# Kernel optimization log

Hardware: AMD Instinct MI355X
Metric: run time of the kernel (lower is better)

The kernel has to match this reference:

```python
import jax, jax.numpy as jnp
import numpy as np

N_SITES = 16
BATCH = 8192
K = 256
EPS = 1e-10


def _entanglement_entropy(sites_A, sites_B):
    # sites_A: [b, pA, k], sites_B: [b, pB, k]
    corr = jnp.einsum('bik,bjk->bij', sites_A, sites_B)  # [b, pA, pB]
    s = jnp.linalg.svd(corr, compute_uv=False)           # [b, min(pA,pB)]
    s_sq = s * s + EPS
    p = s_sq / jnp.sum(s_sq, axis=-1, keepdims=True)
    return -jnp.sum(p * jnp.log(p + EPS), axis=-1)        # [b]


def setup_inputs() -> dict:
    key = jax.random.key(0)
    sites = jax.random.normal(key, (BATCH, N_SITES, K), dtype=jnp.float32)
    return {"sites": sites}


def reference(sites) -> jnp.ndarray:
    # sites: [batch, n_sites, k]; list-of-tensors in the original, stacked here.
    n = sites.shape[1]
    mid = n // 2  # 8
    # Whole-system bipartition
    S_whole = _entanglement_entropy(sites[:, :mid], sites[:, mid:])
    # Left half bipartition (mid_left = mid // 2 = 4)
    ml = mid // 2
    S_left = _entanglement_entropy(sites[:, :ml], sites[:, ml:mid])
    # Right half bipartition
    nr = n - mid
    mr = nr // 2
    S_right = _entanglement_entropy(sites[:, mid:mid + mr], sites[:, mid + mr:])
    phi_q = S_whole - (S_left + S_right)
    return jax.nn.relu(phi_q)
```

## Files before the change

### kernel.cpp

```cpp
#include <hip/hip_runtime.h>
#include <math.h>

#define DEV __device__ __forceinline__

DEV float rcp_fast(float x) { return __builtin_amdgcn_rcpf(x); }
DEV float rsq_fast(float x) { return __builtin_amdgcn_rsqf(x); }

__host__ __device__ constexpr int TI(int n, int i, int j) {
  return n * i - (i * (i - 1)) / 2 + (j - i);
}

template <int N>
DEV float& sym_at(float (&a)[N * (N + 1) / 2], int i, int j) {
  return (i <= j) ? a[TI(N, i, j)] : a[TI(N, j, i)];
}

template <int N>
DEV void pivot_params(float (&a)[N * (N + 1) / 2], int p, int q,
                      float& c_out, float& s_out) {
  float apq = a[TI(N, p, q)];
  float app = a[TI(N, p, p)];
  float aqq = a[TI(N, q, q)];
  float h = aqq - app;
  float tw = apq + apq;
  float den = fabsf(h) + sqrtf(fmaf(h, h, tw * tw)) + 1e-37f;
  float t = tw * rcp_fast(den);
  t = (h < 0.0f) ? -t : t;
  float c = rsq_fast(fmaf(t, t, 1.0f));
  float s = t * c;
  c_out = c;
  s_out = s;
  a[TI(N, p, p)] = fmaf(-t, apq, app);
  a[TI(N, q, q)] = fmaf( t, apq, aqq);
  a[TI(N, p, q)] = 0.0f;
}

template <int N>
DEV void cross_update(float (&a)[N * (N + 1) / 2], int pa, int qa, int pb,
                      int qb, float ca, float sa, float cb, float sb) {
  float w = sym_at<N>(a, pa, pb), x = sym_at<N>(a, pa, qb);
  float y = sym_at<N>(a, qa, pb), z = sym_at<N>(a, qa, qb);
  float w1 = fmaf(ca, w, -sa * y), x1 = fmaf(ca, x, -sa * z);
  float y1 = fmaf(sa, w,  ca * y), z1 = fmaf(sa, x,  ca * z);
  sym_at<N>(a, pa, pb) = fmaf(cb, w1, -sb * x1);
  sym_at<N>(a, pa, qb) = fmaf(sb, w1,  cb * x1);
  sym_at<N>(a, qa, pb) = fmaf(cb, y1, -sb * z1);
  sym_at<N>(a, qa, qb) = fmaf(sb, y1,  cb * z1);
}

template <int SW8, int SW4>
DEV void jacobi_fused(float (&W)[36], float (&L)[10], float (&R)[10]) {
  constexpr int P8[7][4][2] = {
      {{0, 7}, {1, 6}, {2, 5}, {3, 4}}, {{0, 1}, {2, 7}, {3, 6}, {4, 5}},
      {{0, 2}, {1, 3}, {4, 7}, {5, 6}}, {{0, 3}, {2, 4}, {1, 5}, {6, 7}},
      {{0, 4}, {3, 5}, {2, 6}, {1, 7}}, {{0, 5}, {4, 6}, {3, 7}, {1, 2}},
      {{0, 6}, {5, 7}, {1, 4}, {2, 3}}};
  constexpr int P4[3][2][2] = {
      {{0, 3}, {1, 2}}, {{0, 1}, {2, 3}}, {{0, 2}, {1, 3}}};
#pragma unroll
  for (int rr = 0; rr < SW8 * 7; ++rr) {
    const int r = rr % 7;
    const bool do4 = ((rr & 1) == 0) && ((rr >> 1) < SW4 * 3);
    const int q = (rr >> 1) % 3;

    float cc[4], ss[4];
#pragma unroll
    for (int u = 0; u < 4; ++u)
      pivot_params<8>(W, P8[r][u][0], P8[r][u][1], cc[u], ss[u]);

    float ca0, sa0, ca1, sa1, cb0, sb0, cb1, sb1;
    if (do4) {
      pivot_params<4>(L, P4[q][0][0], P4[q][0][1], ca0, sa0);
      pivot_params<4>(R, P4[q][0][0], P4[q][0][1], cb0, sb0);
      pivot_params<4>(L, P4[q][1][0], P4[q][1][1], ca1, sa1);
      pivot_params<4>(R, P4[q][1][0], P4[q][1][1], cb1, sb1);
    }

#pragma unroll
    for (int u = 0; u < 4; ++u) {
#pragma unroll
      for (int v = u + 1; v < 4; ++v) {
        cross_update<8>(W, P8[r][u][0], P8[r][u][1], P8[r][v][0], P8[r][v][1],
                        cc[u], ss[u], cc[v], ss[v]);
      }
    }

    if (do4) {
      cross_update<4>(L, P4[q][0][0], P4[q][0][1], P4[q][1][0], P4[q][1][1],
                      ca0, sa0, ca1, sa1);
      cross_update<4>(R, P4[q][0][0], P4[q][0][1], P4[q][1][0], P4[q][1][1],
                      cb0, sb0, cb1, sb1);
    }
  }
}

template <int N>
DEV float entropy_of(const float (&a)[N * (N + 1) / 2]) {
  float lam[N];
  float sum = 0.0f;
#pragma unroll
  for (int i = 0; i < N; ++i) {
    float l = fmaxf(a[TI(N, i, i)], 0.0f) + 1e-10f;
    lam[i] = l;
    sum += l;
  }
  float inv = 1.0f / sum;
  float H = 0.0f;
#pragma unroll
  for (int i = 0; i < N; ++i) {
    float p = lam[i] * inv;
    H = fmaf(p, __logf(p + 1e-10f), H);
  }
  return -H;
}

DEV float reduce_dist_64(float (&cur)[64], int lane) {
#pragma unroll
  for (int d = 0; d < 6; ++d) {
    const int dist = 1 << d;
    const int up = (lane >> d) & 1;
#pragma unroll
    for (int m = 0; m < (64 >> (d + 1)); ++m) {
      float snd = up ? cur[2 * m]     : cur[2 * m + 1];
      float kp  = up ? cur[2 * m + 1] : cur[2 * m];
      float r = __shfl_xor(snd, dist, 64);
      cur[m] = kp + r;
    }
  }
  return cur[0];
}

DEV float reduce_dist_32(float (&cur)[32], int lane) {
#pragma unroll
  for (int d = 0; d < 5; ++d) {
    const int dist = 1 << d;
    const int up = (lane >> d) & 1;
#pragma unroll
    for (int m = 0; m < (32 >> (d + 1)); ++m) {
      float snd = up ? cur[2 * m]     : cur[2 * m + 1];
      float kp  = up ? cur[2 * m + 1] : cur[2 * m];
      float r = __shfl_xor(snd, dist, 64);
      cur[m] = kp + r;
    }
  }
  float v = cur[0];
  v += __shfl_xor(v, 32, 64);
  return v;
}

__global__ __launch_bounds__(64) void corr_kernel(
    const float* __restrict__ sites, float* __restrict__ cmat) {
  const int b = blockIdx.x;
  const int lane = threadIdx.x;
  const float4* base = reinterpret_cast<const float4*>(sites) + (size_t)b * 1024;

  float4 v[16];
#pragma unroll
  for (int s = 0; s < 16; ++s) v[s] = base[s * 64 + lane];

  float aw[64];
#pragma unroll
  for (int i = 0; i < 8; ++i) {
#pragma unroll
    for (int j = 0; j < 8; ++j) {
      float4 a = v[i], c = v[8 + j];
      aw[i * 8 + j] =
          fmaf(a.x, c.x, fmaf(a.y, c.y, fmaf(a.z, c.z, a.w * c.w)));
    }
  }
  float cw = reduce_dist_64(aw, lane);

  float alr[32];
#pragma unroll
  for (int i = 0; i < 4; ++i) {
#pragma unroll
    for (int j = 0; j < 4; ++j) {
      float4 a = v[i], c = v[4 + j];
      alr[i * 4 + j] =
          fmaf(a.x, c.x, fmaf(a.y, c.y, fmaf(a.z, c.z, a.w * c.w)));
      float4 a2 = v[8 + i], c2 = v[12 + j];
      alr[16 + i * 4 + j] =
          fmaf(a2.x, c2.x, fmaf(a2.y, c2.y, fmaf(a2.z, c2.z, a2.w * c2.w)));
    }
  }
  float clr = reduce_dist_32(alr, lane);

  float* row = cmat + (size_t)b * 96;
  row[lane] = cw;
  if (lane < 32) row[64 + lane] = clr;
}

__global__ __launch_bounds__(64) void phi_kernel(
    const float* __restrict__ cmat, float* __restrict__ out) {
  __shared__ float4 lds[64 * 25];
  const int t = threadIdx.x;
  const int b0 = blockIdx.x * 64;

  const float4* src = reinterpret_cast<const float4*>(cmat) + (size_t)b0 * 24;
#pragma unroll
  for (int r = 0; r < 24; ++r) {
    int q = r * 64 + t;
    float4 val = src[q];
    int bl = q / 24;
    int e4 = q - bl * 24;
    lds[bl * 25 + e4] = val;
  }
  __syncthreads();

  const float4* myrow = &lds[t * 25];
  float Cw[64], Cl[16], Cr[16];
#pragma unroll
  for (int j = 0; j < 16; ++j) {
    float4 f = myrow[j];
    Cw[4 * j] = f.x; Cw[4 * j + 1] = f.y; Cw[4 * j + 2] = f.z; Cw[4 * j + 3] = f.w;
  }
#pragma unroll
  for (int j = 0; j < 4; ++j) {
    float4 f = myrow[16 + j];
    Cl[4 * j] = f.x; Cl[4 * j + 1] = f.y; Cl[4 * j + 2] = f.z; Cl[4 * j + 3] = f.w;
    float4 g = myrow[20 + j];
    Cr[4 * j] = g.x; Cr[4 * j + 1] = g.y; Cr[4 * j + 2] = g.z; Cr[4 * j + 3] = g.w;
  }

  float Mw[36];
#pragma unroll
  for (int i = 0; i < 8; ++i) {
#pragma unroll
    for (int j = i; j < 8; ++j) {
      float acc = 0.0f;
#pragma unroll
      for (int k = 0; k < 8; ++k) acc = fmaf(Cw[i * 8 + k], Cw[j * 8 + k], acc);
      Mw[TI(8, i, j)] = acc;
    }
  }
  float Ml[10], Mr[10];
#pragma unroll
  for (int i = 0; i < 4; ++i) {
#pragma unroll
    for (int j = i; j < 4; ++j) {
      float accl = 0.0f, accr = 0.0f;
#pragma unroll
      for (int k = 0; k < 4; ++k) {
        accl = fmaf(Cl[i * 4 + k], Cl[j * 4 + k], accl);
        accr = fmaf(Cr[i * 4 + k], Cr[j * 4 + k], accr);
      }
      Ml[TI(4, i, j)] = accl;
      Mr[TI(4, i, j)] = accr;
    }
  }

  jacobi_fused<3, 3>(Mw, Ml, Mr);

  float Sw = entropy_of<8>(Mw);
  float Sl = entropy_of<4>(Ml);
  float Sr = entropy_of<4>(Mr);

  out[b0 + t] = fmaxf(Sw - Sl - Sr, 0.0f);
}

extern "C" void kernel_launch(void* const* d_in, const int* in_sizes, int n_in,
                              void* d_out, int out_size, void* d_ws, size_t ws_size,
                              hipStream_t stream) {
  const float* sites = (const float*)d_in[0];
  float* out = (float*)d_out;
  float* cmat = (float*)d_ws;

  corr_kernel<<<8192, 64, 0, stream>>>(sites, cmat);
  phi_kernel<<<128, 64, 0, stream>>>(cmat, out);
}
```

Before: 207.6 us.

## Parallelize per-batch Jacobi eigensolve across four lanes with shuffle-based rotations

The phi kernel now assigns four lanes per batch element instead of one. Each lane holds a pair of rows of the 8x8 Gram matrix and rotation parameters are exchanged with wave shuffles, and rows migrate between lanes in a round-robin ordering. The 4x4 left and right problems are handled by lane pairs the same way. The grid grows from 128 to 512 blocks to fill more compute units, at the cost of many cross-lane shuffles and per-lane redundant arithmetic.

```diff
diff --git a/kernel.cpp b/kernel.cpp
--- a/kernel.cpp
+++ b/kernel.cpp
@@ -6,112 +6,125 @@
 DEV float rcp_fast(float x) { return __builtin_amdgcn_rcpf(x); }
 DEV float rsq_fast(float x) { return __builtin_amdgcn_rsqf(x); }
 
-__host__ __device__ constexpr int TI(int n, int i, int j) {
-  return n * i - (i * (i - 1)) / 2 + (j - i);
-}
-
-template <int N>
-DEV float& sym_at(float (&a)[N * (N + 1) / 2], int i, int j) {
-  return (i <= j) ? a[TI(N, i, j)] : a[TI(N, j, i)];
-}
-
-template <int N>
-DEV void pivot_params(float (&a)[N * (N + 1) / 2], int p, int q,
-                      float& c_out, float& s_out) {
-  float apq = a[TI(N, p, q)];
-  float app = a[TI(N, p, p)];
-  float aqq = a[TI(N, q, q)];
+
+DEV void jac_pivot(float app, float apq, float aqq, float& c, float& s) {
   float h = aqq - app;
   float tw = apq + apq;
   float den = fabsf(h) + sqrtf(fmaf(h, h, tw * tw)) + 1e-37f;
   float t = tw * rcp_fast(den);
   t = (h < 0.0f) ? -t : t;
-  float c = rsq_fast(fmaf(t, t, 1.0f));
-  float s = t * c;
-  c_out = c;
-  s_out = s;
-  a[TI(N, p, p)] = fmaf(-t, apq, app);
-  a[TI(N, q, q)] = fmaf( t, apq, aqq);
-  a[TI(N, p, q)] = 0.0f;
-}
-
-template <int N>
-DEV void cross_update(float (&a)[N * (N + 1) / 2], int pa, int qa, int pb,
-                      int qb, float ca, float sa, float cb, float sb) {
-  float w = sym_at<N>(a, pa, pb), x = sym_at<N>(a, pa, qb);
-  float y = sym_at<N>(a, qa, pb), z = sym_at<N>(a, qa, qb);
-  float w1 = fmaf(ca, w, -sa * y), x1 = fmaf(ca, x, -sa * z);
-  float y1 = fmaf(sa, w,  ca * y), z1 = fmaf(sa, x,  ca * z);
-  sym_at<N>(a, pa, pb) = fmaf(cb, w1, -sb * x1);
-  sym_at<N>(a, pa, qb) = fmaf(sb, w1,  cb * x1);
-  sym_at<N>(a, qa, pb) = fmaf(cb, y1, -sb * z1);
-  sym_at<N>(a, qa, qb) = fmaf(sb, y1,  cb * z1);
-}
-
-template <int SW8, int SW4>
-DEV void jacobi_fused(float (&W)[36], float (&L)[10], float (&R)[10]) {
-  constexpr int P8[7][4][2] = {
-      {{0, 7}, {1, 6}, {2, 5}, {3, 4}}, {{0, 1}, {2, 7}, {3, 6}, {4, 5}},
-      {{0, 2}, {1, 3}, {4, 7}, {5, 6}}, {{0, 3}, {2, 4}, {1, 5}, {6, 7}},
-      {{0, 4}, {3, 5}, {2, 6}, {1, 7}}, {{0, 5}, {4, 6}, {3, 7}, {1, 2}},
-      {{0, 6}, {5, 7}, {1, 4}, {2, 3}}};
-  constexpr int P4[3][2][2] = {
-      {{0, 3}, {1, 2}}, {{0, 1}, {2, 3}}, {{0, 2}, {1, 3}}};
-#pragma unroll
-  for (int rr = 0; rr < SW8 * 7; ++rr) {
-    const int r = rr % 7;
-    const bool do4 = ((rr & 1) == 0) && ((rr >> 1) < SW4 * 3);
-    const int q = (rr >> 1) % 3;
-
-    float cc[4], ss[4];
-#pragma unroll
-    for (int u = 0; u < 4; ++u)
-      pivot_params<8>(W, P8[r][u][0], P8[r][u][1], cc[u], ss[u]);
-
-    float ca0, sa0, ca1, sa1, cb0, sb0, cb1, sb1;
-    if (do4) {
-      pivot_params<4>(L, P4[q][0][0], P4[q][0][1], ca0, sa0);
-      pivot_params<4>(R, P4[q][0][0], P4[q][0][1], cb0, sb0);
-      pivot_params<4>(L, P4[q][1][0], P4[q][1][1], ca1, sa1);
-      pivot_params<4>(R, P4[q][1][0], P4[q][1][1], cb1, sb1);
-    }
-
-#pragma unroll
-    for (int u = 0; u < 4; ++u) {
-#pragma unroll
-      for (int v = u + 1; v < 4; ++v) {
-        cross_update<8>(W, P8[r][u][0], P8[r][u][1], P8[r][v][0], P8[r][v][1],
-                        cc[u], ss[u], cc[v], ss[v]);
-      }
-    }
-
-    if (do4) {
-      cross_update<4>(L, P4[q][0][0], P4[q][0][1], P4[q][1][0], P4[q][1][1],
-                      ca0, sa0, ca1, sa1);
-      cross_update<4>(R, P4[q][0][0], P4[q][0][1], P4[q][1][0], P4[q][1][1],
-                      cb0, sb0, cb1, sb1);
-    }
-  }
-}
-
-template <int N>
-DEV float entropy_of(const float (&a)[N * (N + 1) / 2]) {
-  float lam[N];
-  float sum = 0.0f;
-#pragma unroll
-  for (int i = 0; i < N; ++i) {
-    float l = fmaxf(a[TI(N, i, i)], 0.0f) + 1e-10f;
-    lam[i] = l;
-    sum += l;
-  }
-  float inv = 1.0f / sum;
-  float H = 0.0f;
-#pragma unroll
-  for (int i = 0; i < N; ++i) {
-    float p = lam[i] * inv;
-    H = fmaf(p, __logf(p + 1e-10f), H);
-  }
-  return -H;
+  c = rsq_fast(fmaf(t, t, 1.0f));
+  s = t * c;
+}
+
+DEV void w_round(float (&rT)[8], float (&rB)[8], int u, int gbase) {
+  const bool q0 = (u & 1) != 0, q1 = (u & 2) != 0;
+  float appA = q0 ? rT[2] : rT[0], appB = q0 ? rT[6] : rT[4];
+  float app = q1 ? appB : appA;
+  float apqA = q0 ? rT[3] : rT[1], apqB = q0 ? rT[7] : rT[5];
+  float apq = q1 ? apqB : apqA;
+  float aqqA = q0 ? rB[3] : rB[1], aqqB = q0 ? rB[7] : rB[5];
+  float aqq = q1 ? aqqB : aqqA;
+
+  float c, s;
+  jac_pivot(app, apq, aqq, c, s);
+
+#pragma unroll
+  for (int j = 0; j < 8; ++j) {
+    float x = rT[j], y = rB[j];
+    rT[j] = fmaf(c, x, -s * y);
+    rB[j] = fmaf(s, x, c * y);
+  }
+#pragma unroll
+  for (int v = 0; v < 4; ++v) {
+    float cv = __shfl(c, gbase + v, 64);
+    float sv = __shfl(s, gbase + v, 64);
+    float x = rT[2 * v], y = rT[2 * v + 1];
+    rT[2 * v] = fmaf(cv, x, -sv * y);
+    rT[2 * v + 1] = fmaf(sv, x, cv * y);
+    float x2 = rB[2 * v], y2 = rB[2 * v + 1];
+    rB[2 * v] = fmaf(cv, x2, -sv * y2);
+    rB[2 * v + 1] = fmaf(sv, x2, cv * y2);
+  }
+}
+
+DEV void w_migrate(float (&rT)[8], float (&rB)[8], int u, int gbase) {
+  constexpr int SRC[8] = {0, 2, 4, 1, 6, 3, 7, 5};
+  const int upLane = gbase + ((u + 1) & 3);
+  const int dnLane = gbase + ((u + 3) & 3);
+  const bool u0 = (u == 0), u3 = (u == 3);
+  float nT[8], nB[8];
+#pragma unroll
+  for (int sdst = 0; sdst < 8; ++sdst) {
+    const int j = SRC[sdst];
+    float tsh = __shfl(rT[j], upLane, 64);
+    float bsh = __shfl(rB[j], dnLane, 64);
+    nT[sdst] = u0 ? rT[j] : (u3 ? rB[j] : tsh);
+    nB[sdst] = u0 ? tsh : bsh;
+  }
+#pragma unroll
+  for (int sdst = 0; sdst < 8; ++sdst) { rT[sdst] = nT[sdst]; rB[sdst] = nB[sdst]; }
+}
+
+DEV void h_round(float (&rT)[4], float (&rB)[4], int w, int base2) {
+  float app = w ? rT[2] : rT[0];
+  float apq = w ? rT[3] : rT[1];
+  float aqq = w ? rB[3] : rB[1];
+  float c, s;
+  jac_pivot(app, apq, aqq, c, s);
+#pragma unroll
+  for (int j = 0; j < 4; ++j) {
+    float x = rT[j], y = rB[j];
+    rT[j] = fmaf(c, x, -s * y);
+    rB[j] = fmaf(s, x, c * y);
+  }
+#pragma unroll
+  for (int v = 0; v < 2; ++v) {
+    float cv = __shfl(c, base2 + v, 64);
+    float sv = __shfl(s, base2 + v, 64);
+    float x = rT[2 * v], y = rT[2 * v + 1];
+    rT[2 * v] = fmaf(cv, x, -sv * y);
+    rT[2 * v + 1] = fmaf(sv, x, cv * y);
+    float x2 = rB[2 * v], y2 = rB[2 * v + 1];
+    rB[2 * v] = fmaf(cv, x2, -sv * y2);
+    rB[2 * v + 1] = fmaf(sv, x2, cv * y2);
+  }
+}
+
+DEV void h_migrate(float (&rT)[4], float (&rB)[4], int w) {
+  constexpr int SRC[4] = {0, 2, 3, 1};
+  const bool w0 = (w == 0);
+  float nT[4], nB[4];
+#pragma unroll
+  for (int sdst = 0; sdst < 4; ++sdst) {
+    const int j = SRC[sdst];
+    float snd = w0 ? rB[j] : rT[j];
+    float got = __shfl_xor(snd, 1, 64);
+    nT[sdst] = w0 ? rT[j] : rB[j];
+    nB[sdst] = got;
+  }
+#pragma unroll
+  for (int sdst = 0; sdst < 4; ++sdst) { rT[sdst] = nT[sdst]; rB[sdst] = nB[sdst]; }
+}
+
+DEV float dot8(const float (&A)[8], float4 c0, float4 c1) {
+  float acc = A[0] * c0.x;
+  acc = fmaf(A[1], c0.y, acc);
+  acc = fmaf(A[2], c0.z, acc);
+  acc = fmaf(A[3], c0.w, acc);
+  acc = fmaf(A[4], c1.x, acc);
+  acc = fmaf(A[5], c1.y, acc);
+  acc = fmaf(A[6], c1.z, acc);
+  acc = fmaf(A[7], c1.w, acc);
+  return acc;
+}
+
+DEV float dot4(const float (&A)[4], float4 c0) {
+  float acc = A[0] * c0.x;
+  acc = fmaf(A[1], c0.y, acc);
+  acc = fmaf(A[2], c0.z, acc);
+  acc = fmaf(A[3], c0.w, acc);
+  return acc;
 }
 
 DEV float reduce_dist_64(float (&cur)[64], int lane) {
@@ -192,70 +205,107 @@
 
 __global__ __launch_bounds__(64) void phi_kernel(
     const float* __restrict__ cmat, float* __restrict__ out) {
-  __shared__ float4 lds[64 * 25];
+  __shared__ float4 lds4[16 * 25];
   const int t = threadIdx.x;
-  const int b0 = blockIdx.x * 64;
+  const int b0 = blockIdx.x * 16;
 
   const float4* src = reinterpret_cast<const float4*>(cmat) + (size_t)b0 * 24;
 #pragma unroll
-  for (int r = 0; r < 24; ++r) {
+  for (int r = 0; r < 6; ++r) {
     int q = r * 64 + t;
     float4 val = src[q];
     int bl = q / 24;
     int e4 = q - bl * 24;
-    lds[bl * 25 + e4] = val;
+    lds4[bl * 25 + e4] = val;
   }
   __syncthreads();
 
-  const float4* myrow = &lds[t * 25];
-  float Cw[64], Cl[16], Cr[16];
-#pragma unroll
-  for (int j = 0; j < 16; ++j) {
-    float4 f = myrow[j];
-    Cw[4 * j] = f.x; Cw[4 * j + 1] = f.y; Cw[4 * j + 2] = f.z; Cw[4 * j + 3] = f.w;
-  }
-#pragma unroll
-  for (int j = 0; j < 4; ++j) {
-    float4 f = myrow[16 + j];
-    Cl[4 * j] = f.x; Cl[4 * j + 1] = f.y; Cl[4 * j + 2] = f.z; Cl[4 * j + 3] = f.w;
-    float4 g = myrow[20 + j];
-    Cr[4 * j] = g.x; Cr[4 * j + 1] = g.y; Cr[4 * j + 2] = g.z; Cr[4 * j + 3] = g.w;
-  }
-
-  float Mw[36];
-#pragma unroll
-  for (int i = 0; i < 8; ++i) {
-#pragma unroll
-    for (int j = i; j < 8; ++j) {
-      float acc = 0.0f;
-#pragma unroll
-      for (int k = 0; k < 8; ++k) acc = fmaf(Cw[i * 8 + k], Cw[j * 8 + k], acc);
-      Mw[TI(8, i, j)] = acc;
-    }
-  }
-  float Ml[10], Mr[10];
-#pragma unroll
-  for (int i = 0; i < 4; ++i) {
-#pragma unroll
-    for (int j = i; j < 4; ++j) {
-      float accl = 0.0f, accr = 0.0f;
-#pragma unroll
-      for (int k = 0; k < 4; ++k) {
-        accl = fmaf(Cl[i * 4 + k], Cl[j * 4 + k], accl);
-        accr = fmaf(Cr[i * 4 + k], Cr[j * 4 + k], accr);
-      }
-      Ml[TI(4, i, j)] = accl;
-      Mr[TI(4, i, j)] = accr;
-    }
-  }
-
-  jacobi_fused<3, 3>(Mw, Ml, Mr);
-
-  float Sw = entropy_of<8>(Mw);
-  float Sl = entropy_of<4>(Ml);
-  float Sr = entropy_of<4>(Mr);
-
-  out[b0 + t] = fmaxf(Sw - Sl - Sr, 0.0f);
+  const int u = t & 3;
+  const int grp = t >> 2;
+  const int gbase = t & ~3;
+  const int base2 = t & ~1;
+  const int w = u & 1;
+  const float* Crow = reinterpret_cast<const float*>(lds4) + grp * 100;
+
+  float Cp[8], Cq[8];
+  {
+    const float4* P = reinterpret_cast<const float4*>(Crow + u * 8);
+    float4 a0 = P[0], a1 = P[1];
+    Cp[0] = a0.x; Cp[1] = a0.y; Cp[2] = a0.z; Cp[3] = a0.w;
+    Cp[4] = a1.x; Cp[5] = a1.y; Cp[6] = a1.z; Cp[7] = a1.w;
+    const float4* Q = reinterpret_cast<const float4*>(Crow + (7 - u) * 8);
+    float4 e0 = Q[0], e1 = Q[1];
+    Cq[0] = e0.x; Cq[1] = e0.y; Cq[2] = e0.z; Cq[3] = e0.w;
+    Cq[4] = e1.x; Cq[5] = e1.y; Cq[6] = e1.z; Cq[7] = e1.w;
+  }
+  float rT[8], rB[8];
+#pragma unroll
+  for (int sl = 0; sl < 8; ++sl) {
+    const int j = (sl & 1) ? (7 - (sl >> 1)) : (sl >> 1);
+    const float4* J = reinterpret_cast<const float4*>(Crow + j * 8);
+    float4 c0 = J[0], c1 = J[1];
+    rT[sl] = dot8(Cp, c0, c1);
+    rB[sl] = dot8(Cq, c0, c1);
+  }
+
+  const int cbase = 64 + ((u >> 1) << 4);
+  float Dp[4], Dq[4];
+  {
+    float4 dp = *reinterpret_cast<const float4*>(Crow + cbase + w * 4);
+    float4 dq = *reinterpret_cast<const float4*>(Crow + cbase + (3 - w) * 4);
+    Dp[0] = dp.x; Dp[1] = dp.y; Dp[2] = dp.z; Dp[3] = dp.w;
+    Dq[0] = dq.x; Dq[1] = dq.y; Dq[2] = dq.z; Dq[3] = dq.w;
+  }
+  float rT4[4], rB4[4];
+#pragma unroll
+  for (int sl = 0; sl < 4; ++sl) {
+    const int j = (sl & 1) ? (3 - (sl >> 1)) : (sl >> 1);
+    float4 cj = *reinterpret_cast<const float4*>(Crow + cbase + j * 4);
+    rT4[sl] = dot4(Dp, cj);
+    rB4[sl] = dot4(Dq, cj);
+  }
+
+#pragma unroll
+  for (int rr = 0; rr < 21; ++rr) {
+    w_round(rT, rB, u, gbase);
+    if ((rr & 1) == 0 && rr < 18) {
+      h_round(rT4, rB4, w, base2);
+      h_migrate(rT4, rB4, w);
+    }
+    w_migrate(rT, rB, u, gbase);
+  }
+
+  const bool q0 = (u & 1) != 0, q1 = (u & 2) != 0;
+  float eTa = q0 ? rT[2] : rT[0], eTb = q0 ? rT[6] : rT[4];
+  float lT = q1 ? eTb : eTa;
+  float eBa = q0 ? rB[3] : rB[1], eBb = q0 ? rB[7] : rB[5];
+  float lB = q1 ? eBb : eBa;
+  lT = fmaxf(lT, 0.0f) + 1e-10f;
+  lB = fmaxf(lB, 0.0f) + 1e-10f;
+  float sm = lT + lB;
+  sm += __shfl_xor(sm, 1, 64);
+  sm += __shfl_xor(sm, 2, 64);
+  float inv = 1.0f / sm;
+  float pT = lT * inv, pB = lB * inv;
+  float hh = fmaf(pT, __logf(pT + 1e-10f), pB * __logf(pB + 1e-10f));
+  hh += __shfl_xor(hh, 1, 64);
+  hh += __shfl_xor(hh, 2, 64);
+  float Sw = -hh;
+
+  float l0 = w ? rT4[2] : rT4[0];
+  float l1 = w ? rB4[3] : rB4[1];
+  l0 = fmaxf(l0, 0.0f) + 1e-10f;
+  l1 = fmaxf(l1, 0.0f) + 1e-10f;
+  float s4 = l0 + l1;
+  s4 += __shfl_xor(s4, 1, 64);
+  float i4 = 1.0f / s4;
+  float p0 = l0 * i4, p1 = l1 * i4;
+  float h4 = fmaf(p0, __logf(p0 + 1e-10f), p1 * __logf(p1 + 1e-10f));
+  h4 += __shfl_xor(h4, 1, 64);
+  float S4 = -h4;
+  float So = __shfl_xor(S4, 2, 64);
+  float phi = fmaxf(Sw - S4 - So, 0.0f);
+  if (u == 0) out[b0 + grp] = phi;
 }
 
 extern "C" void kernel_launch(void* const* d_in, const int* in_sizes, int n_in,
@@ -266,5 +316,5 @@
   float* cmat = (float*)d_ws;
 
   corr_kernel<<<8192, 64, 0, stream>>>(sites, cmat);
-  phi_kernel<<<128, 64, 0, stream>>>(cmat, out);
-}
+  phi_kernel<<<512, 64, 0, stream>>>(cmat, out);
+}
```

New measurement: 205.9 us. Within noise of the previous version (-0.8%).
